# Performance work log

Measured on AMD Instinct MI355X. Metric: run time of the kernel, lower is better.

## Reference

```python
import jax, jax.numpy as jnp
import numpy as np

EMBED_DIM = 1024
NUM_HEADS = 16


def setup_inputs() -> dict:
    key = jax.random.key(0)
    kx, kq, kk, kv, ko = jax.random.split(key, 5)
    B, S, D = 2, 2048, EMBED_DIM
    s = 1.0 / np.sqrt(D)
    return {
        "x": jax.random.normal(kx, (B, S, D), dtype=jnp.float32),
        "Wq": jax.random.normal(kq, (D, D), dtype=jnp.float32) * s,
        "Wk": jax.random.normal(kk, (D, D), dtype=jnp.float32) * s,
        "Wv": jax.random.normal(kv, (D, D), dtype=jnp.float32) * s,
        "Wo": jax.random.normal(ko, (D, D), dtype=jnp.float32) * s,
    }


def reference(x, Wq, Wk, Wv, Wo):
    B, S, D = x.shape
    H = NUM_HEADS
    d_k = D // H
    # QKV projections (nn.Linear applies x @ W.T)
    q = (x @ Wq.T).reshape(B, S, H, d_k).transpose(0, 2, 1, 3)  # [B,H,S,d_k]
    k = (x @ Wk.T).reshape(B, S, H, d_k).transpose(0, 2, 1, 3)
    v = (x @ Wv.T).reshape(B, S, H, d_k).transpose(0, 2, 1, 3)
    scores = jnp.einsum("bhqd,bhkd->bhqk", q, k) / jnp.sqrt(jnp.float32(d_k))
    probs = jax.nn.softmax(scores, axis=-1)  # dropout is identity in eval
    attn = jnp.einsum("bhqk,bhkd->bhqd", probs, v)  # [B,H,S,d_k]
    attn = attn.transpose(0, 2, 1, 3).reshape(B, S, D)
    return attn @ Wo.T
```

## Files before the change

### kernel.cpp

```cpp
#include <hip/hip_runtime.h>
#include <stdint.h>

typedef __attribute__((ext_vector_type(4))) float    f32x4;
typedef __attribute__((ext_vector_type(8))) _Float16 half8;
typedef __attribute__((ext_vector_type(4))) _Float16 half4;
typedef unsigned long long u64;

#define MFMA16(a, b, c)    __builtin_amdgcn_mfma_f32_16x16x32_f16(a, b, c, 0, 0, 0)
#define MFMA16K16(a, b, c) __builtin_amdgcn_mfma_f32_16x16x16f16(a, b, c, 0, 0, 0)

#if __has_builtin(__builtin_amdgcn_exp2f)
#define EXP2F(x) __builtin_amdgcn_exp2f(x)
#else
#define EXP2F(x) exp2f(x)
#endif

#define CEXP 0.18033688f

__device__ inline void gl_lds16(const void* g, void* l) {
    __builtin_amdgcn_global_load_lds(
        (const __attribute__((address_space(1))) unsigned int*)g,
        (__attribute__((address_space(3))) unsigned int*)l, 16, 0, 0);
}

__global__ __launch_bounds__(256) void cast_all(
    const float* __restrict__ x,  const float* __restrict__ wq,
    const float* __restrict__ wk, const float* __restrict__ wv,
    const float* __restrict__ wo,
    _Float16* __restrict__ xh,  _Float16* __restrict__ wqh,
    _Float16* __restrict__ wkh, _Float16* __restrict__ wvh,
    _Float16* __restrict__ woh) {
    const int NX = 4194304, NW = 1048576;
    int i = (blockIdx.x * 256 + threadIdx.x) * 4;
    const float* src; _Float16* dst; int off;
    if (i < NX) { src = x; dst = xh; off = i; }
    else {
        int j = i - NX; int w = j >> 20; off = j & (NW - 1);
        src = (w == 0) ? wq : (w == 1) ? wk : (w == 2) ? wv : wo;
        dst = (w == 0) ? wqh : (w == 1) ? wkh : (w == 2) ? wvh : woh;
    }
    f32x4 v = *(const f32x4*)(src + off);
    half4 o;
    o.x = (_Float16)v.x; o.y = (_Float16)v.y; o.z = (_Float16)v.z; o.w = (_Float16)v.w;
    *(half4*)(dst + off) = o;
}

#define BN 128
#define BK 64

template <int MODE>
__global__ __launch_bounds__(256) void gemm_bt(const _Float16* __restrict__ A,
                                               const _Float16* __restrict__ B,
                                               void* __restrict__ C0,
                                               void* __restrict__ C1,
                                               void* __restrict__ C2,
                                               int M, int N, int K) {
    constexpr int BM  = (MODE == 3) ? 128 : 64;
    constexpr int MT  = BM / 32;
    constexpr int AIT = BM / 32;

    __shared__ __attribute__((aligned(16))) _Float16 smem[(BM + BN) * BK];
    _Float16* As = smem;
    _Float16* Bs = smem + BM * BK;

    const int tid  = threadIdx.x;
    const int wave = tid >> 6;
    const int lane = tid & 63;
    const int l16  = lane & 15;
    const int quad = lane >> 4;
    const int m0 = blockIdx.y * BM;
    const int n0 = blockIdx.x * BN;
    const int wm = (wave >> 1) * (BM / 2);
    const int wn = (wave & 1) * 64;

    const int srow = tid >> 3;
    const int scc  = (tid & 7) ^ ((tid >> 3) & 7);

    f32x4 acc[MT][4];
#pragma unroll
    for (int i = 0; i < MT; i++)
#pragma unroll
        for (int j = 0; j < 4; j++) acc[i][j] = (f32x4){0.f, 0.f, 0.f, 0.f};

    for (int k0 = 0; k0 < K; k0 += BK) {
        __syncthreads();
#pragma unroll
        for (int i = 0; i < AIT; i++)
            gl_lds16(A + (size_t)(m0 + i * 32 + srow) * K + k0 + scc * 8,
                     (char*)As + i * 4096 + wave * 1024);
#pragma unroll
        for (int i = 0; i < 4; i++)
            gl_lds16(B + (size_t)(n0 + i * 32 + srow) * K + k0 + scc * 8,
                     (char*)Bs + i * 4096 + wave * 1024);
        __syncthreads();

#pragma unroll
        for (int kk = 0; kk < 2; kk++) {
            half8 af[MT], bf[4];
#pragma unroll
            for (int mt = 0; mt < MT; mt++) {
                int row = wm + mt * 16 + l16;
                af[mt] = *(const half8*)(As + row * 64 + ((quad + 4 * kk) ^ (row & 7)) * 8);
            }
#pragma unroll
            for (int nt = 0; nt < 4; nt++) {
                int row = wn + nt * 16 + l16;
                bf[nt] = *(const half8*)(Bs + row * 64 + ((quad + 4 * kk) ^ (row & 7)) * 8);
            }
#pragma unroll
            for (int mt = 0; mt < MT; mt++)
#pragma unroll
                for (int nt = 0; nt < 4; nt++)
                    acc[mt][nt] = MFMA16(af[mt], bf[nt], acc[mt][nt]);
        }
    }

    if (MODE == 0) {
        float* C = (float*)C0;
#pragma unroll
        for (int mt = 0; mt < MT; mt++)
#pragma unroll
            for (int r = 0; r < 4; r++) {
                int row = m0 + wm + mt * 16 + quad * 4 + r;
                float* Crow = C + (size_t)row * N + n0 + wn + l16;
#pragma unroll
                for (int nt = 0; nt < 4; nt++) Crow[nt * 16] = acc[mt][nt][r];
            }
    } else {
        const int region = n0 >> 10;
        const int nb = (n0 & 1023) + wn;
        if (region < 2) {
            _Float16* C = (region == 0) ? (_Float16*)C0 : (_Float16*)C1;
            const float scale = (region == 0) ? CEXP : 1.f;
#pragma unroll
            for (int mt = 0; mt < MT; mt++)
#pragma unroll
                for (int r = 0; r < 4; r++) {
                    int mg = m0 + wm + mt * 16 + quad * 4 + r;
                    int b = mg >> 11, s = mg & 2047;
#pragma unroll
                    for (int nt = 0; nt < 4; nt++) {
                        int nw = nb + nt * 16 + l16;
                        int h = nw >> 6, d = nw & 63;
                        C[(((size_t)b * 16 + h) * 2048 + s) * 64 + d] =
                            (_Float16)(acc[mt][nt][r] * scale);
                    }
                }
        } else {
            __syncthreads();
            _Float16* ep = smem + wave * 4096;
#pragma unroll
            for (int mt = 0; mt < MT; mt++)
#pragma unroll
                for (int nt = 0; nt < 4; nt++) {
                    int dn = nt * 16 + l16;
                    int slot = (mt * 2 + (quad >> 1)) ^ (dn & 7);
                    union { half4 h; u64 q; } o;
#pragma unroll
                    for (int r = 0; r < 4; r++) o.h[r] = (_Float16)acc[mt][nt][r];
                    *(u64*)(ep + dn * 64 + slot * 8 + (quad & 1) * 4) = o.q;
                }
            __syncthreads();
            int mgb = m0 + wm;
            int b = mgb >> 11, sbase = mgb & 2047;
            int h = nb >> 6;
            _Float16* C = (_Float16*)C2 + ((size_t)b * 16 + h) * 64 * 2048;
#pragma unroll
            for (int j = 0; j < 8; j++) {
                int dn = j * 8 + (lane >> 3);
                int slot = (lane & 7) ^ (dn & 7);
                half8 val = *(const half8*)(ep + dn * 64 + slot * 8);
                *(half8*)(C + (size_t)dn * 2048 + sbase + (lane & 7) * 8) = val;
            }
        }
    }
}

__global__ __launch_bounds__(256) void attn_kernel(const _Float16* __restrict__ Q,
                                                   const _Float16* __restrict__ Kg,
                                                   const _Float16* __restrict__ Vt,
                                                   _Float16* __restrict__ Oa) {
    __shared__ __attribute__((aligned(16))) _Float16 Ks[64 * 64];
    __shared__ __attribute__((aligned(16))) _Float16 Vs[64 * 68];

    const int tid  = threadIdx.x;
    const int wave = tid >> 6;
    const int lane = tid & 63;
    const int l16  = lane & 15;
    const int quad = lane >> 4;
    const int bh = blockIdx.y;
    const int q0 = blockIdx.x * 128 + wave * 32;

    half8 qf[2][2];
#pragma unroll
    for (int qt = 0; qt < 2; qt++)
#pragma unroll
        for (int kk = 0; kk < 2; kk++)
            qf[qt][kk] = *(const half8*)(Q + ((size_t)bh * 2048 + q0 + qt * 16 + l16) * 64 +
                                         (quad + 4 * kk) * 8);

    const int srow = tid >> 3;
    const int sc8  = tid & 7;
    const int kslot = sc8 ^ (srow & 7);

    const _Float16* kp = Kg + (size_t)bh * 2048 * 64 + (size_t)srow * 64 + sc8 * 8;
    const _Float16* vp = Vt + (size_t)bh * 64 * 2048 + (size_t)srow * 2048 + sc8 * 8;

    f32x4 lsum4[2];
    f32x4 oacc[2][4];
#pragma unroll
    for (int qt = 0; qt < 2; qt++) {
        lsum4[qt] = (f32x4){0.f, 0.f, 0.f, 0.f};
#pragma unroll
        for (int dt = 0; dt < 4; dt++) oacc[qt][dt] = (f32x4){0.f, 0.f, 0.f, 0.f};
    }

    half8 kr0 = *(const half8*)(kp);
    half8 kr1 = *(const half8*)(kp + 32 * 64);
    half8 vr0 = *(const half8*)(vp);
    half8 vr1 = *(const half8*)(vp + 32 * 2048);

    for (int kt = 0; kt < 2048; kt += 64) {
        __syncthreads();
        *(half8*)(Ks + srow * 64 + kslot * 8) = kr0;
        *(half8*)(Ks + (srow + 32) * 64 + kslot * 8) = kr1;
        {
            union { half8 h; u64 q[2]; } u0, u1;
            u0.h = vr0; u1.h = vr1;
            _Float16* vd0 = Vs + srow * 68 + sc8 * 8;
            _Float16* vd1 = Vs + (srow + 32) * 68 + sc8 * 8;
            *(u64*)(vd0) = u0.q[0]; *(u64*)(vd0 + 4) = u0.q[1];
            *(u64*)(vd1) = u1.q[0]; *(u64*)(vd1 + 4) = u1.q[1];
        }
        __syncthreads();

        {
            int kt2 = (kt + 64) & 2047;
            kr0 = *(const half8*)(kp + (size_t)kt2 * 64);
            kr1 = *(const half8*)(kp + (size_t)(kt2 + 32) * 64);
            vr0 = *(const half8*)(vp + kt2);
            vr1 = *(const half8*)(vp + 32 * 2048 + kt2);
        }

        f32x4 sc4[2][4];
#pragma unroll
        for (int nt = 0; nt < 4; nt++) {
            int row = nt * 16 + l16;
            half8 kf0 = *(const half8*)(Ks + row * 64 + (quad ^ (row & 7)) * 8);
            half8 kf1 = *(const half8*)(Ks + row * 64 + ((quad + 4) ^ (row & 7)) * 8);
#pragma unroll
            for (int qt = 0; qt < 2; qt++) {
                f32x4 s = (f32x4){0.f, 0.f, 0.f, 0.f};
                s = MFMA16(kf0, qf[qt][0], s);
                s = MFMA16(kf1, qf[qt][1], s);
                sc4[qt][nt] = s;
            }
        }

        half4 ph[2][4];
#pragma unroll
        for (int qt = 0; qt < 2; qt++)
#pragma unroll
            for (int nt = 0; nt < 4; nt++) {
                half4 p;
#pragma unroll
                for (int r = 0; r < 4; r++) {
                    float pe = EXP2F(sc4[qt][nt][r]);
                    lsum4[qt][r] += pe;
                    p[r] = (_Float16)pe;
                }
                ph[qt][nt] = p;
            }

#pragma unroll
        for (int nt = 0; nt < 4; nt++) {
#pragma unroll
            for (int dt = 0; dt < 4; dt++) {
                int row = dt * 16 + l16;
                half4 vf = *(const half4*)(Vs + row * 68 + nt * 16 + quad * 4);
#pragma unroll
                for (int qt = 0; qt < 2; qt++)
                    oacc[qt][dt] = MFMA16K16(vf, ph[qt][nt], oacc[qt][dt]);
            }
        }
    }

    const int b = bh >> 4, h = bh & 15;
#pragma unroll
    for (int qt = 0; qt < 2; qt++) {
        float ls = (lsum4[qt][0] + lsum4[qt][1]) + (lsum4[qt][2] + lsum4[qt][3]);
        ls += __shfl_xor(ls, 16);
        ls += __shfl_xor(ls, 32);
        float inv = 1.f / ls;
        int q = q0 + qt * 16 + l16;
        _Float16* orow = Oa + ((size_t)b * 2048 + q) * 1024 + h * 64;
#pragma unroll
        for (int dt = 0; dt < 4; dt++) {
            half4 o;
#pragma unroll
            for (int r = 0; r < 4; r++) o[r] = (_Float16)(oacc[qt][dt][r] * inv);
            *(half4*)(orow + dt * 16 + quad * 4) = o;
        }
    }
}

extern "C" void kernel_launch(void* const* d_in, const int* in_sizes, int n_in,
                              void* d_out, int out_size, void* d_ws, size_t ws_size,
                              hipStream_t stream) {
    const float* x  = (const float*)d_in[0];
    const float* Wq = (const float*)d_in[1];
    const float* Wk = (const float*)d_in[2];
    const float* Wv = (const float*)d_in[3];
    const float* Wo = (const float*)d_in[4];
    float* out = (float*)d_out;

    const int NX = 2 * 2048 * 1024;
    const int NW = 1024 * 1024;

    _Float16* ws  = (_Float16*)d_ws;
    _Float16* xh  = ws;
    _Float16* wqh = xh + NX;
    _Float16* wkh = wqh + NW;
    _Float16* wvh = wkh + NW;
    _Float16* woh = wvh + NW;
    _Float16* Qb  = woh + NW;
    _Float16* Kb  = Qb + NX;
    _Float16* Vtb = Kb + NX;
    _Float16* Ab  = Vtb + NX;

    cast_all<<<8192, 256, 0, stream>>>(x, Wq, Wk, Wv, Wo, xh, wqh, wkh, wvh, woh);

    gemm_bt<3><<<dim3(3072 / 128, 4096 / 128), 256, 0, stream>>>(
        xh, wqh, Qb, Kb, Vtb, 4096, 3072, 1024);

    attn_kernel<<<dim3(16, 32), 256, 0, stream>>>(Qb, Kb, Vtb, Ab);

    gemm_bt<0><<<dim3(1024 / 128, 4096 / 64), 256, 0, stream>>>(
        Ab, woh, out, nullptr, nullptr, 4096, 1024, 1024);
}
```

Baseline: 191.8 us.

## Prefetch GEMM tiles through registers; shrink attention query tile with double-buffered LDS

The projection GEMM drops direct global-to-LDS loads and instead loads the next K-slice into registers while the current slice is computed, then writes it into swizzled LDS at the top of the next iteration. The attention kernel now gives each wave 16 query rows instead of 32, which doubles the grid to 1024 blocks. It double-buffers the K/V shared-memory tiles so one barrier per iteration is enough. The aim is to overlap global latency with MFMA work and raise occupancy across CUs. The cost is more register pressure in the GEMM and twice as many K/V reloads per query in attention.

```diff
diff --git a/kernel.cpp b/kernel.cpp
--- a/kernel.cpp
+++ b/kernel.cpp
@@ -16,12 +16,6 @@
 #endif
 
 #define CEXP 0.18033688f
-
-__device__ inline void gl_lds16(const void* g, void* l) {
-    __builtin_amdgcn_global_load_lds(
-        (const __attribute__((address_space(1))) unsigned int*)g,
-        (__attribute__((address_space(3))) unsigned int*)l, 16, 0, 0);
-}
 
 __global__ __launch_bounds__(256) void cast_all(
     const float* __restrict__ x,  const float* __restrict__ wq,
@@ -74,25 +68,39 @@
     const int wn = (wave & 1) * 64;
 
     const int srow = tid >> 3;
-    const int scc  = (tid & 7) ^ ((tid >> 3) & 7);
+    const int g8   = tid & 7;
+    const int slot = g8 ^ (srow & 7);
+
+    const _Float16* Ap = A + (size_t)(m0 + srow) * K + g8 * 8;
+    const _Float16* Bp = B + (size_t)(n0 + srow) * K + g8 * 8;
 
     f32x4 acc[MT][4];
 #pragma unroll
     for (int i = 0; i < MT; i++)
 #pragma unroll
         for (int j = 0; j < 4; j++) acc[i][j] = (f32x4){0.f, 0.f, 0.f, 0.f};
+
+    half8 ar[AIT], br[4];
+#pragma unroll
+    for (int i = 0; i < AIT; i++) ar[i] = *(const half8*)(Ap + (size_t)i * 32 * K);
+#pragma unroll
+    for (int i = 0; i < 4; i++)  br[i] = *(const half8*)(Bp + (size_t)i * 32 * K);
 
     for (int k0 = 0; k0 < K; k0 += BK) {
         __syncthreads();
 #pragma unroll
         for (int i = 0; i < AIT; i++)
-            gl_lds16(A + (size_t)(m0 + i * 32 + srow) * K + k0 + scc * 8,
-                     (char*)As + i * 4096 + wave * 1024);
+            *(half8*)(As + (i * 32 + srow) * 64 + slot * 8) = ar[i];
 #pragma unroll
         for (int i = 0; i < 4; i++)
-            gl_lds16(B + (size_t)(n0 + i * 32 + srow) * K + k0 + scc * 8,
-                     (char*)Bs + i * 4096 + wave * 1024);
+            *(half8*)(Bs + (i * 32 + srow) * 64 + slot * 8) = br[i];
         __syncthreads();
+
+        int k2 = k0 + BK; if (k2 == K) k2 = 0;
+#pragma unroll
+        for (int i = 0; i < AIT; i++) ar[i] = *(const half8*)(Ap + (size_t)i * 32 * K + k2);
+#pragma unroll
+        for (int i = 0; i < 4; i++)  br[i] = *(const half8*)(Bp + (size_t)i * 32 * K + k2);
 
 #pragma unroll
         for (int kk = 0; kk < 2; kk++) {
@@ -154,11 +162,11 @@
 #pragma unroll
                 for (int nt = 0; nt < 4; nt++) {
                     int dn = nt * 16 + l16;
-                    int slot = (mt * 2 + (quad >> 1)) ^ (dn & 7);
+                    int sl = (mt * 2 + (quad >> 1)) ^ (dn & 7);
                     union { half4 h; u64 q; } o;
 #pragma unroll
                     for (int r = 0; r < 4; r++) o.h[r] = (_Float16)acc[mt][nt][r];
-                    *(u64*)(ep + dn * 64 + slot * 8 + (quad & 1) * 4) = o.q;
+                    *(u64*)(ep + dn * 64 + sl * 8 + (quad & 1) * 4) = o.q;
                 }
             __syncthreads();
             int mgb = m0 + wm;
@@ -168,8 +176,8 @@
 #pragma unroll
             for (int j = 0; j < 8; j++) {
                 int dn = j * 8 + (lane >> 3);
-                int slot = (lane & 7) ^ (dn & 7);
-                half8 val = *(const half8*)(ep + dn * 64 + slot * 8);
+                int sl = (lane & 7) ^ (dn & 7);
+                half8 val = *(const half8*)(ep + dn * 64 + sl * 8);
                 *(half8*)(C + (size_t)dn * 2048 + sbase + (lane & 7) * 8) = val;
             }
         }
@@ -180,8 +188,8 @@
                                                    const _Float16* __restrict__ Kg,
                                                    const _Float16* __restrict__ Vt,
                                                    _Float16* __restrict__ Oa) {
-    __shared__ __attribute__((aligned(16))) _Float16 Ks[64 * 64];
-    __shared__ __attribute__((aligned(16))) _Float16 Vs[64 * 68];
+    __shared__ __attribute__((aligned(16))) _Float16 Ks[2][64 * 64];
+    __shared__ __attribute__((aligned(16))) _Float16 Vs[2][64 * 68];
 
     const int tid  = threadIdx.x;
     const int wave = tid >> 6;
@@ -189,31 +197,22 @@
     const int l16  = lane & 15;
     const int quad = lane >> 4;
     const int bh = blockIdx.y;
-    const int q0 = blockIdx.x * 128 + wave * 32;
-
-    half8 qf[2][2];
-#pragma unroll
-    for (int qt = 0; qt < 2; qt++)
-#pragma unroll
-        for (int kk = 0; kk < 2; kk++)
-            qf[qt][kk] = *(const half8*)(Q + ((size_t)bh * 2048 + q0 + qt * 16 + l16) * 64 +
-                                         (quad + 4 * kk) * 8);
-
-    const int srow = tid >> 3;
-    const int sc8  = tid & 7;
-    const int kslot = sc8 ^ (srow & 7);
-
-    const _Float16* kp = Kg + (size_t)bh * 2048 * 64 + (size_t)srow * 64 + sc8 * 8;
-    const _Float16* vp = Vt + (size_t)bh * 64 * 2048 + (size_t)srow * 2048 + sc8 * 8;
-
-    f32x4 lsum4[2];
-    f32x4 oacc[2][4];
-#pragma unroll
-    for (int qt = 0; qt < 2; qt++) {
-        lsum4[qt] = (f32x4){0.f, 0.f, 0.f, 0.f};
-#pragma unroll
-        for (int dt = 0; dt < 4; dt++) oacc[qt][dt] = (f32x4){0.f, 0.f, 0.f, 0.f};
-    }
+    const int q0 = blockIdx.x * 64 + wave * 16;
+
+    half8 qf0 = *(const half8*)(Q + ((size_t)bh * 2048 + q0 + l16) * 64 + quad * 8);
+    half8 qf1 = *(const half8*)(Q + ((size_t)bh * 2048 + q0 + l16) * 64 + (quad + 4) * 8);
+
+    const int srow  = tid >> 3;
+    const int g8    = tid & 7;
+    const int kslot = g8 ^ (srow & 7);
+
+    const _Float16* kp = Kg + (size_t)bh * 2048 * 64 + (size_t)srow * 64 + g8 * 8;
+    const _Float16* vp = Vt + (size_t)bh * 64 * 2048 + (size_t)srow * 2048 + g8 * 8;
+
+    f32x4 lsum4 = (f32x4){0.f, 0.f, 0.f, 0.f};
+    f32x4 oacc[4];
+#pragma unroll
+    for (int dt = 0; dt < 4; dt++) oacc[dt] = (f32x4){0.f, 0.f, 0.f, 0.f};
 
     half8 kr0 = *(const half8*)(kp);
     half8 kr1 = *(const half8*)(kp + 32 * 64);
@@ -221,14 +220,14 @@
     half8 vr1 = *(const half8*)(vp + 32 * 2048);
 
     for (int kt = 0; kt < 2048; kt += 64) {
-        __syncthreads();
-        *(half8*)(Ks + srow * 64 + kslot * 8) = kr0;
-        *(half8*)(Ks + (srow + 32) * 64 + kslot * 8) = kr1;
+        const int p = (kt >> 6) & 1;
+        *(half8*)(&Ks[p][srow * 64 + kslot * 8]) = kr0;
+        *(half8*)(&Ks[p][(srow + 32) * 64 + kslot * 8]) = kr1;
         {
             union { half8 h; u64 q[2]; } u0, u1;
             u0.h = vr0; u1.h = vr1;
-            _Float16* vd0 = Vs + srow * 68 + sc8 * 8;
-            _Float16* vd1 = Vs + (srow + 32) * 68 + sc8 * 8;
+            _Float16* vd0 = &Vs[p][srow * 68 + g8 * 8];
+            _Float16* vd1 = &Vs[p][(srow + 32) * 68 + g8 * 8];
             *(u64*)(vd0) = u0.q[0]; *(u64*)(vd0 + 4) = u0.q[1];
             *(u64*)(vd1) = u1.q[0]; *(u64*)(vd1 + 4) = u1.q[1];
         }
@@ -242,65 +241,55 @@
             vr1 = *(const half8*)(vp + 32 * 2048 + kt2);
         }
 
-        f32x4 sc4[2][4];
+        f32x4 sc4[4];
 #pragma unroll
         for (int nt = 0; nt < 4; nt++) {
             int row = nt * 16 + l16;
-            half8 kf0 = *(const half8*)(Ks + row * 64 + (quad ^ (row & 7)) * 8);
-            half8 kf1 = *(const half8*)(Ks + row * 64 + ((quad + 4) ^ (row & 7)) * 8);
-#pragma unroll
-            for (int qt = 0; qt < 2; qt++) {
-                f32x4 s = (f32x4){0.f, 0.f, 0.f, 0.f};
-                s = MFMA16(kf0, qf[qt][0], s);
-                s = MFMA16(kf1, qf[qt][1], s);
-                sc4[qt][nt] = s;
-            }
-        }
-
-        half4 ph[2][4];
-#pragma unroll
-        for (int qt = 0; qt < 2; qt++)
-#pragma unroll
-            for (int nt = 0; nt < 4; nt++) {
-                half4 p;
-#pragma unroll
-                for (int r = 0; r < 4; r++) {
-                    float pe = EXP2F(sc4[qt][nt][r]);
-                    lsum4[qt][r] += pe;
-                    p[r] = (_Float16)pe;
-                }
-                ph[qt][nt] = p;
-            }
+            half8 kf0 = *(const half8*)(&Ks[p][row * 64 + (quad ^ (row & 7)) * 8]);
+            half8 kf1 = *(const half8*)(&Ks[p][row * 64 + ((quad + 4) ^ (row & 7)) * 8]);
+            f32x4 s = (f32x4){0.f, 0.f, 0.f, 0.f};
+            s = MFMA16(kf0, qf0, s);
+            s = MFMA16(kf1, qf1, s);
+            sc4[nt] = s;
+        }
+
+        half4 ph[4];
+#pragma unroll
+        for (int nt = 0; nt < 4; nt++) {
+            half4 pk;
+#pragma unroll
+            for (int r = 0; r < 4; r++) {
+                float pe = EXP2F(sc4[nt][r]);
+                lsum4[r] += pe;
+                pk[r] = (_Float16)pe;
+            }
+            ph[nt] = pk;
+        }
 
 #pragma unroll
         for (int nt = 0; nt < 4; nt++) {
 #pragma unroll
             for (int dt = 0; dt < 4; dt++) {
                 int row = dt * 16 + l16;
-                half4 vf = *(const half4*)(Vs + row * 68 + nt * 16 + quad * 4);
-#pragma unroll
-                for (int qt = 0; qt < 2; qt++)
-                    oacc[qt][dt] = MFMA16K16(vf, ph[qt][nt], oacc[qt][dt]);
+                half4 vf = *(const half4*)(&Vs[p][row * 68 + nt * 16 + quad * 4]);
+                oacc[dt] = MFMA16K16(vf, ph[nt], oacc[dt]);
             }
         }
     }
 
     const int b = bh >> 4, h = bh & 15;
-#pragma unroll
-    for (int qt = 0; qt < 2; qt++) {
-        float ls = (lsum4[qt][0] + lsum4[qt][1]) + (lsum4[qt][2] + lsum4[qt][3]);
-        ls += __shfl_xor(ls, 16);
-        ls += __shfl_xor(ls, 32);
-        float inv = 1.f / ls;
-        int q = q0 + qt * 16 + l16;
-        _Float16* orow = Oa + ((size_t)b * 2048 + q) * 1024 + h * 64;
-#pragma unroll
-        for (int dt = 0; dt < 4; dt++) {
-            half4 o;
-#pragma unroll
-            for (int r = 0; r < 4; r++) o[r] = (_Float16)(oacc[qt][dt][r] * inv);
-            *(half4*)(orow + dt * 16 + quad * 4) = o;
-        }
+    float ls = (lsum4[0] + lsum4[1]) + (lsum4[2] + lsum4[3]);
+    ls += __shfl_xor(ls, 16);
+    ls += __shfl_xor(ls, 32);
+    float inv = 1.f / ls;
+    int q = q0 + l16;
+    _Float16* orow = Oa + ((size_t)b * 2048 + q) * 1024 + h * 64;
+#pragma unroll
+    for (int dt = 0; dt < 4; dt++) {
+        half4 o;
+#pragma unroll
+        for (int r = 0; r < 4; r++) o[r] = (_Float16)(oacc[dt][r] * inv);
+        *(half4*)(orow + dt * 16 + quad * 4) = o;
     }
 }
 
@@ -333,7 +322,7 @@
     gemm_bt<3><<<dim3(3072 / 128, 4096 / 128), 256, 0, stream>>>(
         xh, wqh, Qb, Kb, Vtb, 4096, 3072, 1024);
 
-    attn_kernel<<<dim3(16, 32), 256, 0, stream>>>(Qb, Kb, Vtb, Ab);
+    attn_kernel<<<dim3(32, 32), 256, 0, stream>>>(Qb, Kb, Vtb, Ab);
 
     gemm_bt<0><<<dim3(1024 / 128, 4096 / 64), 256, 0, stream>>>(
         Ab, woh, out, nullptr, nullptr, 4096, 1024, 1024);
```

Result: slower. 198.4 us (+3.4%).
